# Kernel tuning notes

Hardware: AMD Instinct MI355X
Metric: run time of the kernel (lower is better)

Reference implementation:

```python
import jax, jax.numpy as jnp
import numpy as np

B, C, H, W = 8, 192, 128, 128
E, HID, TOP_K = 4, 384, 2


def setup_inputs() -> dict:
    key = jax.random.key(0)
    ks = jax.random.split(key, 5)
    sn = lambda k, sh, sc: jax.random.normal(k, sh, jnp.float32) * sc
    return {
        "x": jax.random.normal(ks[0], (B, C, H, W), jnp.float32),
        "router_w": sn(ks[1], (E, C), C ** -0.5),
        "router_b": jnp.zeros((E,), jnp.float32),
        "fc1_w": sn(ks[2], (E, HID, C), C ** -0.5),
        "fc1_b": jnp.zeros((E, HID), jnp.float32),
        "fc2_w": sn(ks[3], (E, C, HID), HID ** -0.5),
        "fc2_b": jnp.zeros((E, C), jnp.float32),
        "scale": jnp.array([0.1], jnp.float32),
    }


def reference(x, router_w, router_b, fc1_w, fc1_b, fc2_w, fc2_b, scale):
    b, c, h, w = x.shape
    e = router_w.shape[0]
    # (B,C,H,W) -> (B, N, C) tokens
    tokens = jnp.transpose(x, (0, 2, 3, 1)).reshape(b, h * w, c)
    logits = tokens @ router_w.T + router_b            # (B,N,E)
    topv, topi = jax.lax.top_k(logits, TOP_K)          # (B,N,K)
    wts = jax.nn.softmax(topv, axis=-1)                # (B,N,K)
    # per-expert combine weight: sum_k wts_k * [topi_k == e]  -> (B,N,E)
    gates = jnp.sum(jax.nn.one_hot(topi, e, dtype=tokens.dtype) * wts[..., None], axis=-2)
    out = jnp.zeros_like(tokens)
    for ei in range(e):  # small fixed expert count
        hid = jax.nn.gelu(tokens @ fc1_w[ei].T + fc1_b[ei], approximate=False)
        y_e = hid @ fc2_w[ei].T + fc2_b[ei]
        out = out + gates[..., ei:ei + 1] * y_e
    out = jnp.transpose(out.reshape(b, h, w, c), (0, 3, 1, 2))
    return x + scale[0] * out
```

## Files before the change

### kernel.cpp

```cpp
#include <hip/hip_runtime.h>
#include <stdint.h>

typedef __attribute__((ext_vector_type(4))) float f32x4;
typedef unsigned long long u64;
typedef __attribute__((ext_vector_type(2))) u64 u64x2;

#define CC   192
#define NN   16384
#define EE   4
#define HIDD 384

#define OFF_X    0u
#define OFF_HID  12800u
#define OFF_PART 12800u
#define OFF_OUT  25600u
#define OFF_GATE 76560u
#define OFF_LIST 77584u
#define OFF_CNT  78608u
#define LDS_SZ   78640
#define XROWB    200u
#define OROWB    784u

__device__ __forceinline__ uint32_t fp8b(float f){
  uint32_t u = __builtin_bit_cast(uint32_t, f);
  uint32_t s = (u >> 24) & 0x80u;
  float af = fminf(__builtin_fabsf(f), 448.0f);
  if (af < 0.015625f) return s;
  uint32_t v = __builtin_bit_cast(uint32_t, af);
  v += 0x7FFFFu + ((v >> 20) & 1u);
  uint32_t e = (v >> 23) - 120u;
  return s | (e << 3) | ((v >> 20) & 7u);
}
#if __has_builtin(__builtin_amdgcn_cvt_pk_fp8_f32)
__device__ __forceinline__ uint32_t fp8x4(float a, float b, float c, float d){
  int v = __builtin_amdgcn_cvt_pk_fp8_f32(a, b, 0, false);
  v = __builtin_amdgcn_cvt_pk_fp8_f32(c, d, v, true);
  return (uint32_t)v;
}
#else
__device__ __forceinline__ uint32_t fp8x4(float a, float b, float c, float d){
  return fp8b(a) | (fp8b(b) << 8) | (fp8b(c) << 16) | (fp8b(d) << 24);
}
#endif
__device__ __forceinline__ float gelu_f(float v){
  float e = __builtin_amdgcn_exp2f(v * -2.4554669f);
  return v * __builtin_amdgcn_rcpf(1.0f + e);
}
__device__ __forceinline__ f32x4 mfma8(u64 a, u64 b, f32x4 c){
  asm("v_mfma_f32_16x16x32_fp8_fp8 %0, %1, %2, %0" : "+v"(c) : "v"(a), "v"(b));
  return c;
}

#define WAITV(n) do{ asm volatile("s_waitcnt vmcnt(" #n ")"); \
                     __builtin_amdgcn_sched_barrier(0); }while(0)
#define BARRIER() do{ __builtin_amdgcn_sched_barrier(0); \
                      asm volatile("s_waitcnt lgkmcnt(0)"); \
                      __builtin_amdgcn_s_barrier(); \
                      __builtin_amdgcn_sched_barrier(0); }while(0)

__device__ __forceinline__ void issue_w1(const uint8_t* a0, const uint8_t* a1,
                                         const uint8_t* a2, const float* bb,
                                         u64x2 (&w)[9], f32x4 (&bv)[3]){
  asm volatile(
    "global_load_dwordx4 %0, %[A0], off\n\t"
    "global_load_dwordx4 %1, %[A0], off offset:16\n\t"
    "global_load_dwordx4 %2, %[A0], off offset:32\n\t"
    "global_load_dwordx4 %3, %[A1], off\n\t"
    "global_load_dwordx4 %4, %[A1], off offset:16\n\t"
    "global_load_dwordx4 %5, %[A1], off offset:32\n\t"
    "global_load_dwordx4 %6, %[A2], off\n\t"
    "global_load_dwordx4 %7, %[A2], off offset:16\n\t"
    "global_load_dwordx4 %8, %[A2], off offset:32\n\t"
    "global_load_dwordx4 %9, %[B], off\n\t"
    "global_load_dwordx4 %10, %[B], off offset:64\n\t"
    "global_load_dwordx4 %11, %[B], off offset:128"
    : "=&v"(w[0]), "=&v"(w[1]), "=&v"(w[2]), "=&v"(w[3]), "=&v"(w[4]), "=&v"(w[5]),
      "=&v"(w[6]), "=&v"(w[7]), "=&v"(w[8]), "=&v"(bv[0]), "=&v"(bv[1]), "=&v"(bv[2])
    : [A0]"v"(a0), [A1]"v"(a1), [A2]"v"(a2), [B]"v"(bb));
}
__device__ __forceinline__ void issue_w2(const uint8_t* a0, const uint8_t* a1,
                                         const uint8_t* a2, u64x2 (&w)[9]){
  asm volatile(
    "global_load_dwordx4 %0, %[A0], off\n\t"
    "global_load_dwordx4 %1, %[A0], off offset:16\n\t"
    "global_load_dwordx4 %2, %[A0], off offset:32\n\t"
    "global_load_dwordx4 %3, %[A1], off\n\t"
    "global_load_dwordx4 %4, %[A1], off offset:16\n\t"
    "global_load_dwordx4 %5, %[A1], off offset:32\n\t"
    "global_load_dwordx4 %6, %[A2], off\n\t"
    "global_load_dwordx4 %7, %[A2], off offset:16\n\t"
    "global_load_dwordx4 %8, %[A2], off offset:32"
    : "=&v"(w[0]), "=&v"(w[1]), "=&v"(w[2]), "=&v"(w[3]), "=&v"(w[4]), "=&v"(w[5]),
      "=&v"(w[6]), "=&v"(w[7]), "=&v"(w[8])
    : [A0]"v"(a0), [A1]"v"(a1), [A2]"v"(a2));
}

extern "C" __global__ void kconv(const float* __restrict__ w1, const float* __restrict__ w2,
                                 uint8_t* __restrict__ w1f8, uint8_t* __restrict__ w2f8){
  int i = blockIdx.x * 256 + threadIdx.x;
  {
    int row = i / 192, k = i % 192;
    int o = k >> 3, kk = o >> 2, lg = o & 3, bi = k & 7;
    w1f8[(size_t)row * 192 + lg * 48 + kk * 8 + bi] = (uint8_t)fp8b(w1[i]);
  }
  {
    int row = i / 384, k = i % 384;
    int o = k >> 3, kk = o >> 2, lg = o & 3, bi = k & 7;
    w2f8[(size_t)row * 384 + lg * 96 + kk * 8 + bi] = (uint8_t)fp8b(w2[i]);
  }
}

__global__ __launch_bounds__(256)
__attribute__((amdgpu_waves_per_eu(2, 2)))
void kmoe(const float* __restrict__ x, const float* __restrict__ rw,
          const float* __restrict__ rb, const uint8_t* __restrict__ w1f8,
          const float* __restrict__ b1, const uint8_t* __restrict__ w2f8,
          const float* __restrict__ b2, const float* __restrict__ scp,
          float* __restrict__ out)
{
  __shared__ __align__(16) unsigned char S[LDS_SZ];
  const int tid  = threadIdx.x;
  const int lane = tid & 63;
  const int wv   = tid >> 6;
  const int lq   = lane & 15;
  const int lg   = lane >> 4;
  const int tile = blockIdx.x;
  const int b    = tile >> 8;
  const int n0   = (tile & 255) << 6;
  const float* xb = x + (size_t)b * CC * NN;

  {
    const int t = lane;
    const uint32_t rowbase = (uint32_t)t * XROWB;
    float a0 = 0.f, a1 = 0.f, a2 = 0.f, a3 = 0.f;
    #pragma unroll
    for (int jj = 0; jj < 6; ++jj){
      float v[8];
      #pragma unroll
      for (int j = 0; j < 8; ++j){
        const int c = wv * 48 + jj * 8 + j;
        v[j] = xb[(size_t)c * NN + n0 + t];
        a0 = __builtin_fmaf(v[j], rw[c],          a0);
        a1 = __builtin_fmaf(v[j], rw[CC + c],     a1);
        a2 = __builtin_fmaf(v[j], rw[2 * CC + c], a2);
        a3 = __builtin_fmaf(v[j], rw[3 * CC + c], a3);
      }
      uint2 p;
      p.x = fp8x4(v[0], v[1], v[2], v[3]);
      p.y = fp8x4(v[4], v[5], v[6], v[7]);
      *(uint2*)(S + rowbase + (uint32_t)(wv * 48 + jj * 8)) = p;
    }
    float* pl = (float*)(S + OFF_PART);
    pl[(wv * 4 + 0) * 64 + t] = a0;
    pl[(wv * 4 + 1) * 64 + t] = a1;
    pl[(wv * 4 + 2) * 64 + t] = a2;
    pl[(wv * 4 + 3) * 64 + t] = a3;
  }
  __syncthreads();

  if (tid < 64){
    const int t = tid;
    const float* pl = (const float*)(S + OFF_PART);
    float l0 = rb[0], l1 = rb[1], l2 = rb[2], l3 = rb[3];
    #pragma unroll
    for (int cg = 0; cg < 4; ++cg){
      l0 += pl[(cg * 4 + 0) * 64 + t];
      l1 += pl[(cg * 4 + 1) * 64 + t];
      l2 += pl[(cg * 4 + 2) * 64 + t];
      l3 += pl[(cg * 4 + 3) * 64 + t];
    }
    int i1 = 0; float v1 = l0;
    if (l1 > v1){ v1 = l1; i1 = 1; }
    if (l2 > v1){ v1 = l2; i1 = 2; }
    if (l3 > v1){ v1 = l3; i1 = 3; }
    float v2 = -3.0e38f; int i2 = 0;
    if (i1 != 0){ v2 = l0; i2 = 0; }
    if (i1 != 1 && l1 > v2){ v2 = l1; i2 = 1; }
    if (i1 != 2 && l2 > v2){ v2 = l2; i2 = 2; }
    if (i1 != 3 && l3 > v2){ v2 = l3; i2 = 3; }
    const float ex = __expf(v2 - v1);
    const float ga = 1.0f / (1.0f + ex);
    const float gb = ex * ga;
    float* glw = (float*)(S + OFF_GATE);
    glw[t * 4 + 0] = (i1 == 0) ? ga : ((i2 == 0) ? gb : 0.0f);
    glw[t * 4 + 1] = (i1 == 1) ? ga : ((i2 == 1) ? gb : 0.0f);
    glw[t * 4 + 2] = (i1 == 2) ? ga : ((i2 == 2) ? gb : 0.0f);
    glw[t * 4 + 3] = (i1 == 3) ? ga : ((i2 == 3) ? gb : 0.0f);
    uint32_t* lst = (uint32_t*)(S + OFF_LIST);
    uint32_t* cw  = (uint32_t*)(S + OFF_CNT);
    #pragma unroll
    for (int e = 0; e < 4; ++e){
      const bool mine = (i1 == e) || (i2 == e);
      const u64 msk = __ballot(mine);
      const int cnt = __popcll(msk);
      const int ng  = (cnt + 15) >> 4;
      if (mine){
        const int slot = (int)__popcll(msk & ((1ull << t) - 1ull));
        lst[e * 64 + slot] = (uint32_t)t;
      }
      if (t >= cnt && t < ng * 16) lst[e * 64 + t] = 0u;
      if (t == 0){ cw[e] = (uint32_t)ng; cw[4 + e] = (uint32_t)cnt; }
    }
  }
  __syncthreads();

  const float* gl = (const float*)(S + OFF_GATE);
  const uint32_t* lst = (const uint32_t*)(S + OFF_LIST);
  const int* cw = (const int*)(S + OFF_CNT);
  uint32_t rowh[4];
  #pragma unroll
  for (int np = 0; np < 4; ++np) rowh[np] = OFF_HID + (uint32_t)(16 * np + lq) * XROWB;

  const uint8_t* w1l = w1f8 + (size_t)(wv * 48 + lq) * 192 + lg * 48;
  const uint8_t* w2l = w2f8 + (size_t)(wv * 48 + lq) * 384 + lg * 96;
  const float*   b1l = b1 + wv * 48 + 4 * lg;

  u64x2 W1[9], W2[9];
  f32x4 BV[3];
  f32x4 oacc[3][4];
  #pragma unroll
  for (int m = 0; m < 3; ++m)
    #pragma unroll
    for (int np = 0; np < 4; ++np)
      oacc[m][np] = (f32x4){0.f, 0.f, 0.f, 0.f};

#define ISSUE_W1(p) issue_w1(w1l + (size_t)(p) * 36864, \
                             w1l + (size_t)(p) * 36864 + 16 * 192, \
                             w1l + (size_t)(p) * 36864 + 32 * 192, \
                             b1l + (p) * 192, W1, BV)
#define ISSUE_W2(e, ch) issue_w2(w2l + (size_t)(e) * 73728 + (ch) * 48, \
                                 w2l + (size_t)(e) * 73728 + (ch) * 48 + 16 * 384, \
                                 w2l + (size_t)(e) * 73728 + (ch) * 48 + 32 * 384, W2)
#define LOAD_TOK(tk, e) do{ \
    _Pragma("unroll") \
    for (int np = 0; np < 4; ++np) tk[np] = lst[(e) * 64 + np * 16 + lq]; }while(0)

#define G1_NP(np, tk, hacc) do{ \
    const uint32_t xrow = OFF_X + tk[np] * XROWB; \
    _Pragma("unroll") \
    for (int kk = 0; kk < 6; ++kk){ \
      const u64 xk = *(const u64*)(S + xrow + (uint32_t)(kk * 32 + lg * 8)); \
      _Pragma("unroll") \
      for (int m = 0; m < 3; ++m){ \
        const u64 a = (kk & 1) ? W1[m * 3 + (kk >> 1)].y : W1[m * 3 + (kk >> 1)].x; \
        hacc[m][np] = mfma8(a, xk, hacc[m][np]); \
      } \
    } }while(0)
#define G1_COMP(ng, tk, hacc) do{ \
    _Pragma("unroll") \
    for (int m = 0; m < 3; ++m) \
      _Pragma("unroll") \
      for (int np = 0; np < 4; ++np) hacc[m][np] = BV[m]; \
    __builtin_amdgcn_s_setprio(1); \
    if (0 < (ng)) G1_NP(0, tk, hacc); \
    if (1 < (ng)) G1_NP(1, tk, hacc); \
    if (2 < (ng)) G1_NP(2, tk, hacc); \
    if (3 < (ng)) G1_NP(3, tk, hacc); \
    __builtin_amdgcn_s_setprio(0); }while(0)

#define G2_NP(np) do{ \
    _Pragma("unroll") \
    for (int kk = 0; kk < 6; ++kk){ \
      const u64 hf = *(const u64*)(S + rowh[np] + (uint32_t)(kk * 32 + lg * 8)); \
      _Pragma("unroll") \
      for (int m = 0; m < 3; ++m){ \
        const u64 a = (kk & 1) ? W2[m * 3 + (kk >> 1)].y : W2[m * 3 + (kk >> 1)].x; \
        oacc[m][np] = mfma8(a, hf, oacc[m][np]); \
      } \
    } }while(0)
#define G2_COMP(ng) do{ \
    __builtin_amdgcn_s_setprio(1); \
    if (0 < (ng)) G2_NP(0); \
    if (1 < (ng)) G2_NP(1); \
    if (2 < (ng)) G2_NP(2); \
    if (3 < (ng)) G2_NP(3); \
    __builtin_amdgcn_s_setprio(0); }while(0)

#define GELU_ST(e, ng, ct, tk, hacc) do{ \
    _Pragma("unroll") \
    for (int np = 0; np < 4; ++np){ \
      if (np < (ng)){ \
        const float g = (np * 16 + lq < (ct)) ? gl[tk[np] * 4 + (e)] : 0.0f; \
        _Pragma("unroll") \
        for (int m = 0; m < 3; ++m){ \
          *(uint32_t*)(S + rowh[np] + (uint32_t)(48 * wv + 16 * m + 4 * lg)) = \
            fp8x4(gelu_f(hacc[m][np][0]) * g, gelu_f(hacc[m][np][1]) * g, \
                  gelu_f(hacc[m][np][2]) * g, gelu_f(hacc[m][np][3]) * g); \
        } \
      } \
    } }while(0)

#define SCATTER(e, ng, ct, tk) do{ \
    _Pragma("unroll") \
    for (int np = 0; np < 4; ++np){ \
      if (np < (ng)){ \
        const uint32_t srow = (np * 16 + lq < (ct)) ? tk[np] : 64u; \
        _Pragma("unroll") \
        for (int m = 0; m < 3; ++m){ \
          float* p = (float*)(S + OFF_OUT + srow * OROWB \
                              + (uint32_t)((48 * wv + 16 * m + 4 * lg) * 4)); \
          f32x4 c = *(const f32x4*)p; \
          c += oacc[m][np]; \
          *(f32x4*)p = c; \
        } \
      } \
      _Pragma("unroll") \
      for (int m = 0; m < 3; ++m) oacc[m][np] = (f32x4){0.f, 0.f, 0.f, 0.f}; \
    } }while(0)

  ISSUE_W1(0);
  ISSUE_W2(0, 0);
  {
    f32x4* oz = (f32x4*)(S + OFF_OUT);
    for (int i = tid; i < 65 * 49; i += 256) oz[i] = (f32x4){0.f, 0.f, 0.f, 0.f};
  }
  {
    const int ng = __builtin_amdgcn_readfirstlane(cw[0]);
    const int ct = __builtin_amdgcn_readfirstlane(cw[4]);
    uint32_t tk[4];
    LOAD_TOK(tk, 0);
    WAITV(9);
    f32x4 hacc[3][4];
    G1_COMP(ng, tk, hacc);
    GELU_ST(0, ng, ct, tk, hacc);
    ISSUE_W1(1);
  }
  BARRIER();

  #pragma unroll 1
  for (int i = 0; i < 7; ++i){
    const int e2 = i >> 1;
    const int p1 = i + 1, e1 = p1 >> 1, ch1 = p1 & 1;
    WAITV(12);
    {
      const int ng2 = __builtin_amdgcn_readfirstlane(cw[e2]);
      G2_COMP(ng2);
      if (i & 1){
        const int ct2 = __builtin_amdgcn_readfirstlane(cw[4 + e2]);
        uint32_t tk2[4];
        LOAD_TOK(tk2, e2);
        SCATTER(e2, ng2, ct2, tk2);
      }
    }
    ISSUE_W2(e1, ch1);
    WAITV(9);
    {
      const int ng1 = __builtin_amdgcn_readfirstlane(cw[e1]);
      const int ct1 = __builtin_amdgcn_readfirstlane(cw[4 + e1]);
      uint32_t tk1[4];
      LOAD_TOK(tk1, e1);
      f32x4 hacc[3][4];
      G1_COMP(ng1, tk1, hacc);
      BARRIER();
      GELU_ST(e1, ng1, ct1, tk1, hacc);
    }
    if (i < 6) ISSUE_W1(i + 2);
    BARRIER();
  }

  WAITV(0);
  {
    const int ng = __builtin_amdgcn_readfirstlane(cw[3]);
    const int ct = __builtin_amdgcn_readfirstlane(cw[4 + 3]);
    G2_COMP(ng);
    uint32_t tk[4];
    LOAD_TOK(tk, 3);
    SCATTER(3, ng, ct, tk);
  }
  BARRIER();

  {
    const int t = lane;
    const float sc = scp[0];
    const f32x4 g4 = *(const f32x4*)(S + OFF_GATE + t * 16);
    const float* xbt = xb + n0 + t;
    float* ob = out + (size_t)b * CC * NN + n0 + t;
    #pragma unroll
    for (int j = 0; j < 12; ++j){
      const int c0 = wv * 48 + j * 4;
      const f32x4 v = *(const f32x4*)(S + OFF_OUT + (uint32_t)t * OROWB + c0 * 4);
      #pragma unroll
      for (int r = 0; r < 4; ++r){
        const int c = c0 + r;
        const float bt = __builtin_fmaf(g4[0], b2[c],
                          __builtin_fmaf(g4[1], b2[CC + c],
                           __builtin_fmaf(g4[2], b2[2 * CC + c], g4[3] * b2[3 * CC + c])));
        ob[(size_t)c * NN] = __builtin_fmaf(sc, v[r] + bt, xbt[(size_t)c * NN]);
      }
    }
  }
#undef ISSUE_W1
#undef ISSUE_W2
#undef LOAD_TOK
#undef G1_NP
#undef G1_COMP
#undef G2_NP
#undef G2_COMP
#undef GELU_ST
#undef SCATTER
}

extern "C" void kernel_launch(void* const* d_in, const int* in_sizes, int n_in,
                              void* d_out, int out_size, void* d_ws, size_t ws_size,
                              hipStream_t stream){
  const float* x  = (const float*)d_in[0];
  const float* rw = (const float*)d_in[1];
  const float* rb = (const float*)d_in[2];
  const float* w1 = (const float*)d_in[3];
  const float* b1 = (const float*)d_in[4];
  const float* w2 = (const float*)d_in[5];
  const float* b2 = (const float*)d_in[6];
  const float* sc = (const float*)d_in[7];
  float* out = (float*)d_out;
  uint8_t* w1f8 = (uint8_t*)d_ws;
  uint8_t* w2f8 = w1f8 + 294912;

  hipLaunchKernelGGL(kconv, dim3(1152), dim3(256), 0, stream, w1, w2, w1f8, w2f8);
  hipLaunchKernelGGL(kmoe,  dim3(2048), dim3(256), 0, stream,
                     x, rw, rb, w1f8, b1, w2f8, b2, sc, out);
}
```

Measured before the change: 190.1 us.

## Double-buffer hidden tile in LDS and store output accumulator as bf16

```diff
diff --git a/kernel.cpp b/kernel.cpp
--- a/kernel.cpp
+++ b/kernel.cpp
@@ -11,15 +11,16 @@
 #define HIDD 384
 
 #define OFF_X    0u
-#define OFF_HID  12800u
+#define OFF_H0   12800u
+#define OFF_H1   25600u
 #define OFF_PART 12800u
-#define OFF_OUT  25600u
-#define OFF_GATE 76560u
-#define OFF_LIST 77584u
-#define OFF_CNT  78608u
-#define LDS_SZ   78640
+#define OFF_OUT  38400u
+#define OFF_GATE 63888u
+#define OFF_LIST 64912u
+#define OFF_CNT  65936u
+#define LDS_SZ   65968
 #define XROWB    200u
-#define OROWB    784u
+#define OROWB    392u
 
 __device__ __forceinline__ uint32_t fp8b(float f){
   uint32_t u = __builtin_bit_cast(uint32_t, f);
@@ -42,6 +43,19 @@
   return fp8b(a) | (fp8b(b) << 8) | (fp8b(c) << 16) | (fp8b(d) << 24);
 }
 #endif
+__device__ __forceinline__ uint32_t pkbf(float lo, float hi){
+  uint32_t ul = __builtin_bit_cast(uint32_t, lo);
+  uint32_t uh = __builtin_bit_cast(uint32_t, hi);
+  ul += 0x7FFFu + ((ul >> 16) & 1u);
+  uh += 0x7FFFu + ((uh >> 16) & 1u);
+  return (ul >> 16) | (uh & 0xFFFF0000u);
+}
+__device__ __forceinline__ float upbf_lo(uint32_t u){
+  return __builtin_bit_cast(float, u << 16);
+}
+__device__ __forceinline__ float upbf_hi(uint32_t u){
+  return __builtin_bit_cast(float, u & 0xFFFF0000u);
+}
 __device__ __forceinline__ float gelu_f(float v){
   float e = __builtin_amdgcn_exp2f(v * -2.4554669f);
   return v * __builtin_amdgcn_rcpf(1.0f + e);
@@ -209,7 +223,7 @@
   const int* cw = (const int*)(S + OFF_CNT);
   uint32_t rowh[4];
   #pragma unroll
-  for (int np = 0; np < 4; ++np) rowh[np] = OFF_HID + (uint32_t)(16 * np + lq) * XROWB;
+  for (int np = 0; np < 4; ++np) rowh[np] = (uint32_t)(16 * np + lq) * XROWB;
 
   const uint8_t* w1l = w1f8 + (size_t)(wv * 48 + lq) * 192 + lg * 48;
   const uint8_t* w2l = w2f8 + (size_t)(wv * 48 + lq) * 384 + lg * 96;
@@ -258,50 +272,54 @@
     if (3 < (ng)) G1_NP(3, tk, hacc); \
     __builtin_amdgcn_s_setprio(0); }while(0)
 
-#define G2_NP(np) do{ \
+#define G2_NP(hb, np) do{ \
     _Pragma("unroll") \
     for (int kk = 0; kk < 6; ++kk){ \
-      const u64 hf = *(const u64*)(S + rowh[np] + (uint32_t)(kk * 32 + lg * 8)); \
+      const u64 hf = *(const u64*)(S + (hb) + rowh[np] + (uint32_t)(kk * 32 + lg * 8)); \
       _Pragma("unroll") \
       for (int m = 0; m < 3; ++m){ \
         const u64 a = (kk & 1) ? W2[m * 3 + (kk >> 1)].y : W2[m * 3 + (kk >> 1)].x; \
         oacc[m][np] = mfma8(a, hf, oacc[m][np]); \
       } \
     } }while(0)
-#define G2_COMP(ng) do{ \
+#define G2_COMP(hb, ng) do{ \
     __builtin_amdgcn_s_setprio(1); \
-    if (0 < (ng)) G2_NP(0); \
-    if (1 < (ng)) G2_NP(1); \
-    if (2 < (ng)) G2_NP(2); \
-    if (3 < (ng)) G2_NP(3); \
+    if (0 < (ng)) G2_NP(hb, 0); \
+    if (1 < (ng)) G2_NP(hb, 1); \
+    if (2 < (ng)) G2_NP(hb, 2); \
+    if (3 < (ng)) G2_NP(hb, 3); \
     __builtin_amdgcn_s_setprio(0); }while(0)
 
-#define GELU_ST(e, ng, ct, tk, hacc) do{ \
+#define GELU_ST(hb, e, ng, ct, tk, hacc) do{ \
     _Pragma("unroll") \
     for (int np = 0; np < 4; ++np){ \
       if (np < (ng)){ \
         const float g = (np * 16 + lq < (ct)) ? gl[tk[np] * 4 + (e)] : 0.0f; \
         _Pragma("unroll") \
         for (int m = 0; m < 3; ++m){ \
-          *(uint32_t*)(S + rowh[np] + (uint32_t)(48 * wv + 16 * m + 4 * lg)) = \
+          *(uint32_t*)(S + (hb) + rowh[np] + (uint32_t)(48 * wv + 16 * m + 4 * lg)) = \
             fp8x4(gelu_f(hacc[m][np][0]) * g, gelu_f(hacc[m][np][1]) * g, \
                   gelu_f(hacc[m][np][2]) * g, gelu_f(hacc[m][np][3]) * g); \
         } \
       } \
     } }while(0)
 
-#define SCATTER(e, ng, ct, tk) do{ \
+#define SCATTER(ng, ct, tk) do{ \
     _Pragma("unroll") \
     for (int np = 0; np < 4; ++np){ \
       if (np < (ng)){ \
         const uint32_t srow = (np * 16 + lq < (ct)) ? tk[np] : 64u; \
         _Pragma("unroll") \
         for (int m = 0; m < 3; ++m){ \
-          float* p = (float*)(S + OFF_OUT + srow * OROWB \
-                              + (uint32_t)((48 * wv + 16 * m + 4 * lg) * 4)); \
-          f32x4 c = *(const f32x4*)p; \
-          c += oacc[m][np]; \
-          *(f32x4*)p = c; \
+          uint32_t* p = (uint32_t*)(S + OFF_OUT + srow * OROWB \
+                                    + (uint32_t)((48 * wv + 16 * m + 4 * lg) * 2)); \
+          uint2 c = *(const uint2*)p; \
+          const float c0 = upbf_lo(c.x) + oacc[m][np][0]; \
+          const float c1 = upbf_hi(c.x) + oacc[m][np][1]; \
+          const float c2 = upbf_lo(c.y) + oacc[m][np][2]; \
+          const float c3 = upbf_hi(c.y) + oacc[m][np][3]; \
+          c.x = pkbf(c0, c1); c.y = pkbf(c2, c3); \
+          *(uint2*)p = c; \
         } \
       } \
       _Pragma("unroll") \
@@ -311,8 +329,8 @@
   ISSUE_W1(0);
   ISSUE_W2(0, 0);
   {
-    f32x4* oz = (f32x4*)(S + OFF_OUT);
-    for (int i = tid; i < 65 * 49; i += 256) oz[i] = (f32x4){0.f, 0.f, 0.f, 0.f};
+    uint2* oz = (uint2*)(S + OFF_OUT);
+    for (int i = tid; i < 65 * 49; i += 256) oz[i] = (uint2){0u, 0u};
   }
   {
     const int ng = __builtin_amdgcn_readfirstlane(cw[0]);
@@ -322,24 +340,26 @@
     WAITV(9);
     f32x4 hacc[3][4];
     G1_COMP(ng, tk, hacc);
-    GELU_ST(0, ng, ct, tk, hacc);
+    GELU_ST(OFF_H0, 0, ng, ct, tk, hacc);
     ISSUE_W1(1);
   }
   BARRIER();
 
   #pragma unroll 1
   for (int i = 0; i < 7; ++i){
+    const uint32_t hb_r = (i & 1) ? OFF_H1 : OFF_H0;
+    const uint32_t hb_w = (i & 1) ? OFF_H0 : OFF_H1;
     const int e2 = i >> 1;
     const int p1 = i + 1, e1 = p1 >> 1, ch1 = p1 & 1;
     WAITV(12);
     {
       const int ng2 = __builtin_amdgcn_readfirstlane(cw[e2]);
-      G2_COMP(ng2);
+      G2_COMP(hb_r, ng2);
       if (i & 1){
         const int ct2 = __builtin_amdgcn_readfirstlane(cw[4 + e2]);
         uint32_t tk2[4];
         LOAD_TOK(tk2, e2);
-        SCATTER(e2, ng2, ct2, tk2);
+        SCATTER(ng2, ct2, tk2);
       }
     }
     ISSUE_W2(e1, ch1);
@@ -351,8 +371,7 @@
       LOAD_TOK(tk1, e1);
       f32x4 hacc[3][4];
       G1_COMP(ng1, tk1, hacc);
-      BARRIER();
-      GELU_ST(e1, ng1, ct1, tk1, hacc);
+      GELU_ST(hb_w, e1, ng1, ct1, tk1, hacc);
     }
     if (i < 6) ISSUE_W1(i + 2);
     BARRIER();
@@ -362,10 +381,10 @@
   {
     const int ng = __builtin_amdgcn_readfirstlane(cw[3]);
     const int ct = __builtin_amdgcn_readfirstlane(cw[4 + 3]);
-    G2_COMP(ng);
+    G2_COMP(OFF_H1, ng);
     uint32_t tk[4];
     LOAD_TOK(tk, 3);
-    SCATTER(3, ng, ct, tk);
+    SCATTER(ng, ct, tk);
   }
   BARRIER();
 
@@ -378,7 +397,11 @@
     #pragma unroll
     for (int j = 0; j < 12; ++j){
       const int c0 = wv * 48 + j * 4;
-      const f32x4 v = *(const f32x4*)(S + OFF_OUT + (uint32_t)t * OROWB + c0 * 4);
+      const uint2 pv = *(const uint2*)(S + OFF_OUT + (uint32_t)t * OROWB
+                                       + (uint32_t)(c0 * 2));
+      float v[4];
+      v[0] = upbf_lo(pv.x); v[1] = upbf_hi(pv.x);
+      v[2] = upbf_lo(pv.y); v[3] = upbf_hi(pv.y);
       #pragma unroll
       for (int r = 0; r < 4; ++r){
         const int c = c0 + r;
```

Result: faster. 179.5 us (-5.6%).
